# Optimization experiments

Hardware: AMD Instinct MI355X
Metric: run time of the kernel (lower is better)

## Reference

```python
import jax, jax.numpy as jnp
import numpy as np

N = 800_000
D = 128
S = 64
EPS = 1e-16  # matches torch_geometric softmax denominator epsilon


def setup_inputs() -> dict:
    key = jax.random.key(0)
    k1, k2, k3 = jax.random.split(key, 3)
    x = jax.random.normal(k1, (N, D), dtype=jnp.float32)
    batch = jnp.sort(jax.random.randint(k2, (N,), 0, S, dtype=jnp.int64))
    gate_W = jax.random.normal(k3, (D, 1), dtype=jnp.float32) * (1.0 / np.sqrt(D))
    gate_b = jnp.zeros((1,), dtype=jnp.float32)
    return {"x": x, "batch": batch, "size": S, "gate_W": gate_W, "gate_b": gate_b}


def reference(x, batch, size, gate_W, gate_b):
    # gate = gate_nn(x).view(-1, 1)  -> [N]
    gate = (x @ gate_W + gate_b)[:, 0]
    # segment-wise numerically-stable softmax over nodes of each graph
    seg_max = jax.ops.segment_max(gate, batch, num_segments=size,
                                  indices_are_sorted=True)
    # guard empty segments (-inf max)
    seg_max = jnp.where(jnp.isfinite(seg_max), seg_max, 0.0)
    g = jnp.exp(gate - seg_max[batch])
    denom = jax.ops.segment_sum(g, batch, num_segments=size,
                                indices_are_sorted=True)
    gate_sm = g / (denom[batch] + EPS)          # [N]
    # weighted scatter-add pooling: out[s] = sum_{i in seg s} gate_i * x_i
    out = jax.ops.segment_sum(gate_sm[:, None] * x, batch, num_segments=size,
                              indices_are_sorted=True)  # [S, D]
    return out, gate_sm[:, None]
```

## Files before the change

kernel.cpp:

```cpp
#include <hip/hip_runtime.h>
#include <hip/hip_bf16.h>
#include <math.h>

#define D 128
#define EPS 1e-16f
#define K_SLOTS 6
#define NBLK_A 2048
#define THR_A 256
#define NWAVES (NBLK_A * THR_A / 64)
#define REC_STRIDE 132

__global__ __launch_bounds__(256) void k_fused(const float* __restrict__ x,
        const int* __restrict__ batch,
        const float* __restrict__ W,
        const float* __restrict__ bptr,
        float* __restrict__ gate,
        float* __restrict__ recs,
        int N, int chunk) {
    const int lane = threadIdx.x & 63;
    const int wave = (blockIdx.x * blockDim.x + threadIdx.x) >> 6;
    float* myrec = recs + (size_t)wave * K_SLOTS * REC_STRIDE;

    if (lane == 0) {
        #pragma unroll
        for (int k = 0; k < K_SLOTS; ++k)
            ((int*)myrec)[k * REC_STRIDE] = -1;
    }

    const int i0 = wave * chunk;
    const int i1 = min(N, i0 + chunk);
    if (i0 >= i1) return;

    const float2 w = ((const float2*)W)[lane];
    const float bias = bptr[0];

    float2 acc = make_float2(0.f, 0.f);
    float m = -INFINITY, l = 0.f;
    int cur = batch[i0];
    int cnt = 0;

    auto flush = [&]() {
        int k = (cnt < K_SLOTS) ? cnt : (K_SLOTS - 1);
        float* r = myrec + k * REC_STRIDE;
        if (lane == 0) { ((int*)r)[0] = cur; r[1] = m; r[2] = l; }
        ((float2*)(r + 4))[lane] = acc;
        ++cnt;
        acc = make_float2(0.f, 0.f); m = -INFINITY; l = 0.f;
    };

    auto upd = [&](int b, float g, float2 xv) {
        if (b != cur) { flush(); cur = b; }
        if (g > m) {
            const float s = __expf(m - g);
            l = l * s + 1.f;
            acc.x = acc.x * s + xv.x;
            acc.y = acc.y * s + xv.y;
            m = g;
        } else {
            const float e = __expf(g - m);
            l += e;
            acc.x += e * xv.x;
            acc.y += e * xv.y;
        }
    };

    int i = i0;
    for (; i + 1 < i1; i += 2) {
        const int b0 = batch[i], b1 = batch[i + 1];
        float2 x0 = ((const float2*)(x + (size_t)i       * D))[lane];
        float2 x1 = ((const float2*)(x + (size_t)(i + 1) * D))[lane];
        float p0 = x0.x * w.x + x0.y * w.y;
        float p1 = x1.x * w.x + x1.y * w.y;
        #pragma unroll
        for (int o = 1; o < 64; o <<= 1) {
            p0 += __shfl_xor(p0, o, 64);
            p1 += __shfl_xor(p1, o, 64);
        }
        const float g0 = p0 + bias, g1 = p1 + bias;
        if (lane == 0) *((float2*)(gate + i)) = make_float2(g0, g1);
        upd(b0, g0, x0);
        upd(b1, g1, x1);
    }
    if (i < i1) {
        const int b0 = batch[i];
        float2 x0 = ((const float2*)(x + (size_t)i * D))[lane];
        float p0 = x0.x * w.x + x0.y * w.y;
        #pragma unroll
        for (int o = 1; o < 64; o <<= 1) p0 += __shfl_xor(p0, o, 64);
        const float g0 = p0 + bias;
        if (lane == 0) gate[i] = g0;
        upd(b0, g0, x0);
    }
    flush();
}

__global__ __launch_bounds__(256) void k_segreduce(const float* __restrict__ recs,
        float* __restrict__ segmax, float* __restrict__ denom,
        float* __restrict__ out, int nrec) {
    const int s = blockIdx.x;
    const int tid = threadIdx.x;
    __shared__ int   list[2048];
    __shared__ float scale[2048];
    __shared__ float red[256];
    __shared__ int cnt_sh;
    if (tid == 0) cnt_sh = 0;
    __syncthreads();

    for (int r = tid; r < nrec; r += 256) {
        if (((const int*)recs)[(size_t)r * REC_STRIDE] == s) {
            int p = atomicAdd(&cnt_sh, 1);
            if (p < 2048) list[p] = r;
        }
    }
    __syncthreads();
    const int cnt = min(cnt_sh, 2048);

    float m = -INFINITY;
    for (int t = tid; t < cnt; t += 256)
        m = fmaxf(m, recs[(size_t)list[t] * REC_STRIDE + 1]);
    red[tid] = m; __syncthreads();
    for (int o = 128; o; o >>= 1) {
        if (tid < o) red[tid] = fmaxf(red[tid], red[tid + o]);
        __syncthreads();
    }
    const float M = red[0];
    __syncthreads();

    float z = 0.f;
    for (int t = tid; t < cnt; t += 256) {
        const float* r = recs + (size_t)list[t] * REC_STRIDE;
        const float sc = __expf(r[1] - M);
        scale[t] = sc;
        z += sc * r[2];
    }
    red[tid] = z; __syncthreads();
    for (int o = 128; o; o >>= 1) {
        if (tid < o) red[tid] += red[tid + o];
        __syncthreads();
    }
    const float Z = red[0];
    if (tid == 0) { segmax[s] = isfinite(M) ? M : 0.f; denom[s] = Z; }

    if (tid < D) {
        float a = 0.f;
        for (int t = 0; t < cnt; ++t)
            a += scale[t] * recs[(size_t)list[t] * REC_STRIDE + 4 + tid];
        out[(size_t)s * D + tid] = a / (Z + EPS);
    }
}

__global__ void k_gatesm(const float* __restrict__ gate,
                         const int* __restrict__ batch,
                         const float* __restrict__ segmax,
                         const float* __restrict__ denom,
                         float* __restrict__ gate_sm, int N) {
    int i = blockIdx.x * blockDim.x + threadIdx.x;
    const int stride = gridDim.x * blockDim.x;
    for (; i < N; i += stride) {
        const int b = batch[i];
        gate_sm[i] = __expf(gate[i] - segmax[b]) / (denom[b] + EPS);
    }
}

extern "C" void kernel_launch(void* const* d_in, const int* in_sizes, int n_in,
                              void* d_out, int out_size, void* d_ws, size_t ws_size,
                              hipStream_t stream) {
    const float* x      = (const float*)d_in[0];
    const int*   batch  = (const int*)d_in[1];
    const float* gate_W = (const float*)d_in[3];
    const float* gate_b = (const float*)d_in[4];

    const int N = in_sizes[0] / D;
    const int S = (out_size - N) / D;

    float* out     = (float*)d_out;
    float* gate_sm = (float*)d_out + (size_t)S * D;

    float* gate   = (float*)d_ws;
    float* segmax = gate + N;
    float* denom  = segmax + S;
    size_t off = ((size_t)(N + 2 * S) + 3) & ~(size_t)3;
    float* recs = (float*)d_ws + off;

    int chunk = (N + NWAVES - 1) / NWAVES;
    chunk = (chunk + 1) & ~1;
    const int nrec = NWAVES * K_SLOTS;

    k_fused<<<NBLK_A, THR_A, 0, stream>>>(x, batch, gate_W, gate_b, gate, recs, N, chunk);
    k_segreduce<<<S, 256, 0, stream>>>(recs, segmax, denom, out, nrec);
    k_gatesm<<<512, 256, 0, stream>>>(gate, batch, segmax, denom, gate_sm, N);
}
```

Before: 685.0 us.

## Use half-wave row groups with prefetch and atomic record reduction

The streaming kernel now assigns 32-lane groups to each chunk, so every lane loads a float4 and the gate dot product needs a shorter shuffle reduction. Loads of x and batch are software-prefetched two rows ahead. The per-segment reduction kernel, which scanned every record once per segment, is replaced by an atomicMax pass over order-preserving float keys, an atomicAdd accumulation pass, and a finalize kernel. An init kernel is added to reset the accumulators and record tags. This removes the serial per-segment scan over all records, at the cost of more kernel launches and contended atomics on a small output array.

```diff
diff --git a/kernel.cpp b/kernel.cpp
--- a/kernel.cpp
+++ b/kernel.cpp
@@ -4,11 +4,29 @@
 
 #define D 128
 #define EPS 1e-16f
-#define K_SLOTS 6
+#define K_SLOTS 4
+#define REC_STRIDE 132
 #define NBLK_A 2048
 #define THR_A 256
-#define NWAVES (NBLK_A * THR_A / 64)
-#define REC_STRIDE 132
+#define NVW (NBLK_A * THR_A / 32)
+#define NREC (NVW * K_SLOTS)
+
+__device__ __forceinline__ unsigned f2o(float f) {
+    unsigned u = __float_as_uint(f);
+    return (u & 0x80000000u) ? ~u : (u | 0x80000000u);
+}
+__device__ __forceinline__ float o2f(unsigned o) {
+    return (o & 0x80000000u) ? __uint_as_float(o & 0x7fffffffu) : __uint_as_float(~o);
+}
+
+__global__ void k_init(unsigned* __restrict__ segMkey, float* __restrict__ denomAcc,
+                       float* __restrict__ outAcc, float* __restrict__ recs, int S) {
+    const int t = blockIdx.x * blockDim.x + threadIdx.x;
+    const int stride = gridDim.x * blockDim.x;
+    for (int i = t; i < S; i += stride) { segMkey[i] = 0x007FFFFFu; denomAcc[i] = 0.f; }
+    for (int i = t; i < S * D; i += stride) outAcc[i] = 0.f;
+    for (int r = t; r < NREC; r += stride) ((int*)recs)[(size_t)r * REC_STRIDE] = -1;
+}
 
 __global__ __launch_bounds__(256) void k_fused(const float* __restrict__ x,
         const int* __restrict__ batch,
@@ -17,148 +35,120 @@
         float* __restrict__ gate,
         float* __restrict__ recs,
         int N, int chunk) {
-    const int lane = threadIdx.x & 63;
-    const int wave = (blockIdx.x * blockDim.x + threadIdx.x) >> 6;
-    float* myrec = recs + (size_t)wave * K_SLOTS * REC_STRIDE;
+    const int sub = threadIdx.x & 31;
+    const int v   = (blockIdx.x * blockDim.x + threadIdx.x) >> 5;
+    const int i0  = v * chunk;
+    const int i1  = min(N, i0 + chunk);
+    if (i0 >= i1) return;
+    float* myrec = recs + (size_t)v * K_SLOTS * REC_STRIDE;
 
-    if (lane == 0) {
-        #pragma unroll
-        for (int k = 0; k < K_SLOTS; ++k)
-            ((int*)myrec)[k * REC_STRIDE] = -1;
-    }
-
-    const int i0 = wave * chunk;
-    const int i1 = min(N, i0 + chunk);
-    if (i0 >= i1) return;
-
-    const float2 w = ((const float2*)W)[lane];
+    const float4 w  = ((const float4*)W)[sub];
     const float bias = bptr[0];
 
-    float2 acc = make_float2(0.f, 0.f);
+    float4 acc = make_float4(0.f, 0.f, 0.f, 0.f);
     float m = -INFINITY, l = 0.f;
     int cur = batch[i0];
     int cnt = 0;
 
     auto flush = [&]() {
-        int k = (cnt < K_SLOTS) ? cnt : (K_SLOTS - 1);
-        float* r = myrec + k * REC_STRIDE;
-        if (lane == 0) { ((int*)r)[0] = cur; r[1] = m; r[2] = l; }
-        ((float2*)(r + 4))[lane] = acc;
+        float* r = myrec + min(cnt, K_SLOTS - 1) * REC_STRIDE;
+        if (sub == 0) { ((int*)r)[0] = cur; r[1] = m; r[2] = l; }
+        ((float4*)(r + 4))[sub] = acc;
         ++cnt;
-        acc = make_float2(0.f, 0.f); m = -INFINITY; l = 0.f;
+        acc = make_float4(0.f, 0.f, 0.f, 0.f); m = -INFINITY; l = 0.f;
     };
 
-    auto upd = [&](int b, float g, float2 xv) {
-        if (b != cur) { flush(); cur = b; }
+    const int n = i1 - i0;
+    float4 xc = ((const float4*)(x + (size_t)i0 * D))[sub];
+    int bc = cur;
+    float4 xn = make_float4(0.f, 0.f, 0.f, 0.f);
+    int bn = cur;
+    if (n > 1) {
+        xn = ((const float4*)(x + (size_t)(i0 + 1) * D))[sub];
+        bn = batch[i0 + 1];
+    }
+
+    for (int s = 0; s < n; ++s) {
+        float4 x2 = xn; int b2 = bn;
+        if (s + 2 < n) {
+            x2 = ((const float4*)(x + (size_t)(i0 + s + 2) * D))[sub];
+            b2 = batch[i0 + s + 2];
+        }
+        float p = xc.x * w.x + xc.y * w.y + xc.z * w.z + xc.w * w.w;
+        p += __shfl_xor(p, 1);
+        p += __shfl_xor(p, 2);
+        p += __shfl_xor(p, 4);
+        p += __shfl_xor(p, 8);
+        p += __shfl_xor(p, 16);
+        const float g = p + bias;
+        if (sub == 0) gate[i0 + s] = g;
+
+        if (bc != cur) { flush(); cur = bc; }
         if (g > m) {
-            const float s = __expf(m - g);
-            l = l * s + 1.f;
-            acc.x = acc.x * s + xv.x;
-            acc.y = acc.y * s + xv.y;
+            const float sc = __expf(m - g);
+            l = l * sc + 1.f;
+            acc.x = acc.x * sc + xc.x;
+            acc.y = acc.y * sc + xc.y;
+            acc.z = acc.z * sc + xc.z;
+            acc.w = acc.w * sc + xc.w;
             m = g;
         } else {
             const float e = __expf(g - m);
             l += e;
-            acc.x += e * xv.x;
-            acc.y += e * xv.y;
+            acc.x += e * xc.x;
+            acc.y += e * xc.y;
+            acc.z += e * xc.z;
+            acc.w += e * xc.w;
         }
-    };
-
-    int i = i0;
-    for (; i + 1 < i1; i += 2) {
-        const int b0 = batch[i], b1 = batch[i + 1];
-        float2 x0 = ((const float2*)(x + (size_t)i       * D))[lane];
-        float2 x1 = ((const float2*)(x + (size_t)(i + 1) * D))[lane];
-        float p0 = x0.x * w.x + x0.y * w.y;
-        float p1 = x1.x * w.x + x1.y * w.y;
-        #pragma unroll
-        for (int o = 1; o < 64; o <<= 1) {
-            p0 += __shfl_xor(p0, o, 64);
-            p1 += __shfl_xor(p1, o, 64);
-        }
-        const float g0 = p0 + bias, g1 = p1 + bias;
-        if (lane == 0) *((float2*)(gate + i)) = make_float2(g0, g1);
-        upd(b0, g0, x0);
-        upd(b1, g1, x1);
-    }
-    if (i < i1) {
-        const int b0 = batch[i];
-        float2 x0 = ((const float2*)(x + (size_t)i * D))[lane];
-        float p0 = x0.x * w.x + x0.y * w.y;
-        #pragma unroll
-        for (int o = 1; o < 64; o <<= 1) p0 += __shfl_xor(p0, o, 64);
-        const float g0 = p0 + bias;
-        if (lane == 0) gate[i] = g0;
-        upd(b0, g0, x0);
+        xc = xn; bc = bn; xn = x2; bn = b2;
     }
     flush();
 }
 
-__global__ __launch_bounds__(256) void k_segreduce(const float* __restrict__ recs,
-        float* __restrict__ segmax, float* __restrict__ denom,
-        float* __restrict__ out, int nrec) {
-    const int s = blockIdx.x;
-    const int tid = threadIdx.x;
-    __shared__ int   list[2048];
-    __shared__ float scale[2048];
-    __shared__ float red[256];
-    __shared__ int cnt_sh;
-    if (tid == 0) cnt_sh = 0;
-    __syncthreads();
+__global__ void k_max(const float* __restrict__ recs, unsigned* __restrict__ segMkey) {
+    const int t = blockIdx.x * blockDim.x + threadIdx.x;
+    const int stride = gridDim.x * blockDim.x;
+    for (int r = t; r < NREC; r += stride) {
+        const float* rec = recs + (size_t)r * REC_STRIDE;
+        const int seg = ((const int*)rec)[0];
+        if (seg >= 0) atomicMax(&segMkey[seg], f2o(rec[1]));
+    }
+}
 
-    for (int r = tid; r < nrec; r += 256) {
-        if (((const int*)recs)[(size_t)r * REC_STRIDE] == s) {
-            int p = atomicAdd(&cnt_sh, 1);
-            if (p < 2048) list[p] = r;
-        }
+__global__ void k_acc(const float* __restrict__ recs,
+                      const unsigned* __restrict__ segMkey,
+                      float* __restrict__ denomAcc, float* __restrict__ outAcc) {
+    const int lane = threadIdx.x & 63;
+    const int wid  = (blockIdx.x * blockDim.x + threadIdx.x) >> 6;
+    const int nw   = (gridDim.x * blockDim.x) >> 6;
+    for (int r = wid; r < NREC; r += nw) {
+        const float* rec = recs + (size_t)r * REC_STRIDE;
+        const int seg = ((const int*)rec)[0];
+        if (seg < 0) continue;
+        const float sc = __expf(rec[1] - o2f(segMkey[seg]));
+        if (lane == 0) atomicAdd(&denomAcc[seg], sc * rec[2]);
+        const float2 a = ((const float2*)(rec + 4))[lane];
+        atomicAdd(&outAcc[(size_t)seg * D + 2 * lane],     sc * a.x);
+        atomicAdd(&outAcc[(size_t)seg * D + 2 * lane + 1], sc * a.y);
     }
-    __syncthreads();
-    const int cnt = min(cnt_sh, 2048);
+}
 
-    float m = -INFINITY;
-    for (int t = tid; t < cnt; t += 256)
-        m = fmaxf(m, recs[(size_t)list[t] * REC_STRIDE + 1]);
-    red[tid] = m; __syncthreads();
-    for (int o = 128; o; o >>= 1) {
-        if (tid < o) red[tid] = fmaxf(red[tid], red[tid + o]);
-        __syncthreads();
-    }
-    const float M = red[0];
-    __syncthreads();
-
-    float z = 0.f;
-    for (int t = tid; t < cnt; t += 256) {
-        const float* r = recs + (size_t)list[t] * REC_STRIDE;
-        const float sc = __expf(r[1] - M);
-        scale[t] = sc;
-        z += sc * r[2];
-    }
-    red[tid] = z; __syncthreads();
-    for (int o = 128; o; o >>= 1) {
-        if (tid < o) red[tid] += red[tid + o];
-        __syncthreads();
-    }
-    const float Z = red[0];
-    if (tid == 0) { segmax[s] = isfinite(M) ? M : 0.f; denom[s] = Z; }
-
-    if (tid < D) {
-        float a = 0.f;
-        for (int t = 0; t < cnt; ++t)
-            a += scale[t] * recs[(size_t)list[t] * REC_STRIDE + 4 + tid];
-        out[(size_t)s * D + tid] = a / (Z + EPS);
-    }
+__global__ void k_fin(const float* __restrict__ outAcc, const float* __restrict__ denomAcc,
+                      float* __restrict__ out, int SD) {
+    const int t = blockIdx.x * blockDim.x + threadIdx.x;
+    if (t < SD) out[t] = outAcc[t] / (denomAcc[t >> 7] + EPS);
 }
 
 __global__ void k_gatesm(const float* __restrict__ gate,
                          const int* __restrict__ batch,
-                         const float* __restrict__ segmax,
-                         const float* __restrict__ denom,
+                         const unsigned* __restrict__ segMkey,
+                         const float* __restrict__ denomAcc,
                          float* __restrict__ gate_sm, int N) {
     int i = blockIdx.x * blockDim.x + threadIdx.x;
     const int stride = gridDim.x * blockDim.x;
     for (; i < N; i += stride) {
         const int b = batch[i];
-        gate_sm[i] = __expf(gate[i] - segmax[b]) / (denom[b] + EPS);
+        gate_sm[i] = __expf(gate[i] - o2f(segMkey[b])) / (denomAcc[b] + EPS);
     }
 }
 
@@ -176,17 +166,19 @@
     float* out     = (float*)d_out;
     float* gate_sm = (float*)d_out + (size_t)S * D;
 
-    float* gate   = (float*)d_ws;
-    float* segmax = gate + N;
-    float* denom  = segmax + S;
-    size_t off = ((size_t)(N + 2 * S) + 3) & ~(size_t)3;
-    float* recs = (float*)d_ws + off;
+    float*    gate     = (float*)d_ws;
+    unsigned* segMkey  = (unsigned*)(gate + N);
+    float*    denomAcc = (float*)(segMkey + S);
+    float*    outAcc   = denomAcc + S;
+    size_t off = ((size_t)(N + 2 * S + S * D) + 3) & ~(size_t)3;
+    float*    recs     = (float*)d_ws + off;
 
-    int chunk = (N + NWAVES - 1) / NWAVES;
-    chunk = (chunk + 1) & ~1;
-    const int nrec = NWAVES * K_SLOTS;
+    int chunk = (N + NVW - 1) / NVW;
 
+    k_init<<<64, 256, 0, stream>>>(segMkey, denomAcc, outAcc, recs, S);
     k_fused<<<NBLK_A, THR_A, 0, stream>>>(x, batch, gate_W, gate_b, gate, recs, N, chunk);
-    k_segreduce<<<S, 256, 0, stream>>>(recs, segmax, denom, out, nrec);
-    k_gatesm<<<512, 256, 0, stream>>>(gate, batch, segmax, denom, gate_sm, N);
+    k_max<<<256, 256, 0, stream>>>(recs, segMkey);
+    k_acc<<<1024, 256, 0, stream>>>(recs, segMkey, denomAcc, outAcc);
+    k_fin<<<(S * D + 255) / 256, 256, 0, stream>>>(outAcc, denomAcc, out, S * D);
+    k_gatesm<<<512, 256, 0, stream>>>(gate, batch, segMkey, denomAcc, gate_sm, N);
 }
```

Result: slower. 775.4 us (+13.2%).
